# Optimization experiments

Measured on AMD Instinct MI355X. Metric: run time of the kernel, lower is better.

Reference implementation:

```python
import jax, jax.numpy as jnp
import numpy as np

N_NODES = 200000
D_IN = 256
D_OUT = 256
B = 4096
K1 = 25   # layer-1 fanout
K2 = 10   # layer-2 fanout
M = B * (1 + K2)  # layer-1 node set size: batch centers + their sampled neighbors


def setup_inputs() -> dict:
    key = jax.random.key(0)
    k1, k2, k3, k4, k5, k6 = jax.random.split(key, 6)
    features = jax.random.normal(k1, (N_NODES, D_IN), dtype=jnp.float32)
    # SageLayer weights: [out, 2*in] (concat path, gcn=False); small kaiming-like scale
    W1 = jax.random.normal(k2, (D_OUT, 2 * D_IN), dtype=jnp.float32) * 0.05
    W2 = jax.random.normal(k3, (D_OUT, 2 * D_OUT), dtype=jnp.float32) * 0.05
    nodes_batch = jax.random.randint(k4, (B,), 0, N_NODES, dtype=jnp.int64)
    neigh2 = jax.random.randint(k5, (B, K2), 0, N_NODES, dtype=jnp.int64)
    neigh1 = jax.random.randint(k6, (M, K1), 0, N_NODES, dtype=jnp.int64)
    return {"features": features, "W1": W1, "W2": W2,
            "nodes_batch": nodes_batch, "neigh2": neigh2, "neigh1": neigh1}


def reference(features, W1, W2, nodes_batch, neigh2, neigh1):
    # Layer-1 node set: centers first, then their sampled layer-2 neighbors.
    l1_nodes = jnp.concatenate([nodes_batch, neigh2.reshape(-1)])  # [M]
    # ---- layer 1: MEAN aggregate over K1 sampled neighbors (gather + mean) ----
    agg1 = jnp.mean(features[neigh1], axis=1)          # [M, K1, D_IN] -> [M, D_IN]
    self1 = features[l1_nodes]                         # [M, D_IN]
    # SageLayer: relu(W.mm(cat(self, agg).T)).T == relu(cat @ W.T)
    h1 = jax.nn.relu(jnp.concatenate([self1, agg1], axis=1) @ W1.T)  # [M, D_OUT]
    # ---- layer 2: centers are h1[:B]; neighbor embeddings are h1[B:] in blocks of K2 ----
    nb = nodes_batch.shape[0]
    agg2 = jnp.mean(h1[nb:].reshape(nb, -1, h1.shape[1]), axis=1)    # [B, D_OUT]
    h2 = jax.nn.relu(jnp.concatenate([h1[:nb], agg2], axis=1) @ W2.T)  # [B, D_OUT]
    return h2
```

## Files before the change

### kernel.cpp

```cpp
#include <hip/hip_runtime.h>
#include <hip/hip_bf16.h>

typedef __attribute__((ext_vector_type(8))) short bf16x8;
typedef __attribute__((ext_vector_type(4))) float f32x4;

#define B_SZ   4096
#define K1     25
#define K2     10
#define M_L1   45056
#define D      256
#define K_DIM  512

static __device__ __forceinline__ unsigned short f2bf(float f) {
    union { float f; unsigned u; } v; v.f = f;
    return (unsigned short)((v.u + 0x7fffu + ((v.u >> 16) & 1u)) >> 16);
}
static __device__ __forceinline__ float bf2f(unsigned short h) {
    union { unsigned u; float f; } v; v.u = ((unsigned)h) << 16;
    return v.f;
}

__global__ __launch_bounds__(256)
void convert_w(const float* __restrict__ W1, const float* __restrict__ W2,
               unsigned short* __restrict__ W1b, unsigned short* __restrict__ W2b) {
    const int i = blockIdx.x * 256 + threadIdx.x;
    W1b[i] = f2bf(W1[i]);
    W2b[i] = f2bf(W2[i]);
}

__global__ __launch_bounds__(256)
void agg1_kernel(const float* __restrict__ feat,
                 const int* __restrict__ nodes_batch,
                 const int* __restrict__ neigh2,
                 const int* __restrict__ neigh1,
                 unsigned short* __restrict__ X1) {
    const int wave = threadIdx.x >> 6;
    const int lane = threadIdx.x & 63;
    const int m = (blockIdx.x << 2) + wave;
    const int self_node = (m < B_SZ) ? nodes_batch[m] : neigh2[m - B_SZ];
    const float4 s = *(const float4*)(feat + (size_t)self_node * D + (lane << 2));
    float sx = 0.f, sy = 0.f, sz = 0.f, sw = 0.f;
    const int* nb = neigh1 + (size_t)m * K1;
    #pragma unroll
    for (int k = 0; k < K1; ++k) {
        const float4 v = *(const float4*)(feat + (size_t)nb[k] * D + (lane << 2));
        sx += v.x; sy += v.y; sz += v.z; sw += v.w;
    }
    const float inv = 1.0f / (float)K1;
    unsigned short* xr = X1 + (size_t)m * K_DIM;
    *(ushort4*)(xr + (lane << 2)) = make_ushort4(f2bf(s.x), f2bf(s.y), f2bf(s.z), f2bf(s.w));
    *(ushort4*)(xr + D + (lane << 2)) =
        make_ushort4(f2bf(sx * inv), f2bf(sy * inv), f2bf(sz * inv), f2bf(sw * inv));
}

__global__ __launch_bounds__(256)
void agg2_kernel(const unsigned short* __restrict__ h1,
                 unsigned short* __restrict__ X2) {
    const int wave = threadIdx.x >> 6;
    const int lane = threadIdx.x & 63;
    const int b = (blockIdx.x << 2) + wave;
    const ushort4 s = *(const ushort4*)(h1 + (size_t)b * D + (lane << 2));
    float sx = 0.f, sy = 0.f, sz = 0.f, sw = 0.f;
    #pragma unroll
    for (int k = 0; k < K2; ++k) {
        const ushort4 v = *(const ushort4*)(h1 + (size_t)(B_SZ + b * K2 + k) * D + (lane << 2));
        sx += bf2f(v.x); sy += bf2f(v.y); sz += bf2f(v.z); sw += bf2f(v.w);
    }
    const float inv = 1.0f / (float)K2;
    unsigned short* xr = X2 + (size_t)b * K_DIM;
    *(ushort4*)(xr + (lane << 2)) = s;
    *(ushort4*)(xr + D + (lane << 2)) =
        make_ushort4(f2bf(sx * inv), f2bf(sy * inv), f2bf(sz * inv), f2bf(sw * inv));
}

template<bool OUT_BF16>
__global__ __launch_bounds__(256)
void gemm_relu(const unsigned short* __restrict__ A,
               const unsigned short* __restrict__ W,
               void* __restrict__ Cout) {
    constexpr int LDA = 40;
    __shared__ unsigned short As[128 * LDA];
    __shared__ unsigned short Bs[128 * LDA];
    const int tid  = threadIdx.x;
    const int wave = tid >> 6, lane = tid & 63;
    const int quad = lane >> 4, l16 = lane & 15;
    const int wm = (wave >> 1) << 6;
    const int wn = (wave & 1) << 6;
    const size_t row0 = (size_t)blockIdx.x * 128;
    const size_t col0 = (size_t)blockIdx.y * 128;
    const int r0 = tid >> 2;
    const int c0 = (tid & 3) << 3;

    f32x4 acc[4][4];
    #pragma unroll
    for (int i = 0; i < 4; ++i)
        #pragma unroll
        for (int j = 0; j < 4; ++j)
            acc[i][j] = (f32x4){0.f, 0.f, 0.f, 0.f};

    const unsigned short* aBase = A + (row0 + r0) * K_DIM + c0;
    const unsigned short* wBase = W + (col0 + r0) * K_DIM + c0;

    for (int k0 = 0; k0 < K_DIM; k0 += 32) {
        __syncthreads();
        *(uint4*)&As[r0 * LDA + c0]        = *(const uint4*)(aBase + k0);
        *(uint4*)&As[(64 + r0) * LDA + c0] = *(const uint4*)(aBase + (size_t)64 * K_DIM + k0);
        *(uint4*)&Bs[r0 * LDA + c0]        = *(const uint4*)(wBase + k0);
        *(uint4*)&Bs[(64 + r0) * LDA + c0] = *(const uint4*)(wBase + (size_t)64 * K_DIM + k0);
        __syncthreads();
        bf16x8 af[4], bfr[4];
        #pragma unroll
        for (int i = 0; i < 4; ++i)
            af[i] = *(const bf16x8*)&As[(wm + i * 16 + l16) * LDA + quad * 8];
        #pragma unroll
        for (int i = 0; i < 4; ++i)
            bfr[i] = *(const bf16x8*)&Bs[(wn + i * 16 + l16) * LDA + quad * 8];
        #pragma unroll
        for (int mi = 0; mi < 4; ++mi)
            #pragma unroll
            for (int ni = 0; ni < 4; ++ni)
                acc[mi][ni] = __builtin_amdgcn_mfma_f32_16x16x32_bf16(
                    af[mi], bfr[ni], acc[mi][ni], 0, 0, 0);
    }

    #pragma unroll
    for (int mi = 0; mi < 4; ++mi) {
        #pragma unroll
        for (int ni = 0; ni < 4; ++ni) {
            #pragma unroll
            for (int r = 0; r < 4; ++r) {
                const size_t gm = row0 + wm + mi * 16 + quad * 4 + r;
                const size_t gn = col0 + wn + ni * 16 + l16;
                float v = acc[mi][ni][r];
                v = v > 0.f ? v : 0.f;
                if (OUT_BF16)
                    ((unsigned short*)Cout)[gm * D + gn] = f2bf(v);
                else
                    ((float*)Cout)[gm * D + gn] = v;
            }
        }
    }
}

extern "C" void kernel_launch(void* const* d_in, const int* in_sizes, int n_in,
                              void* d_out, int out_size, void* d_ws, size_t ws_size,
                              hipStream_t stream) {
    const float* feat        = (const float*)d_in[0];
    const float* W1          = (const float*)d_in[1];
    const float* W2          = (const float*)d_in[2];
    const int*   nodes_batch = (const int*)d_in[3];
    const int*   neigh2      = (const int*)d_in[4];
    const int*   neigh1      = (const int*)d_in[5];
    float* out = (float*)d_out;

    char* ws = (char*)d_ws;
    unsigned short* W1b = (unsigned short*)(ws);
    unsigned short* W2b = (unsigned short*)(ws + 262144);
    unsigned short* X1  = (unsigned short*)(ws + 524288);
    unsigned short* h1  = (unsigned short*)(ws + 524288 + 46137344);
    unsigned short* X2  = (unsigned short*)(ws + 524288 + 46137344 + 23068672);

    convert_w<<<512, 256, 0, stream>>>(W1, W2, W1b, W2b);
    agg1_kernel<<<M_L1 / 4, 256, 0, stream>>>(feat, nodes_batch, neigh2, neigh1, X1);
    gemm_relu<true><<<dim3(M_L1 / 128, 2), 256, 0, stream>>>(X1, W1b, h1);
    agg2_kernel<<<B_SZ / 4, 256, 0, stream>>>(h1, X2);
    gemm_relu<false><<<dim3(B_SZ / 128, 2), 256, 0, stream>>>(X2, W2b, out);
}
```

Before: 455.8 us.

## Convert feature table to bf16 and gather bf16 rows in agg1

Adds a pass that converts the whole fp32 feature table to bf16 in the workspace. agg1 then gathers 512-byte bf16 rows with half-waves, splits neighbors between the two halves, and combines the partial sums with a shuffle. The goal is to halve the bytes moved by the random gather. The cost is a full read of the 200k x 256 fp32 table and a write of its bf16 copy on every call, plus bf16 rounding of the neighbor values before averaging.

```diff
diff --git a/kernel.cpp b/kernel.cpp
--- a/kernel.cpp
+++ b/kernel.cpp
@@ -10,6 +10,7 @@
 #define M_L1   45056
 #define D      256
 #define K_DIM  512
+#define N_NODES 200000
 
 static __device__ __forceinline__ unsigned short f2bf(float f) {
     union { float f; unsigned u; } v; v.f = f;
@@ -18,6 +19,25 @@
 static __device__ __forceinline__ float bf2f(unsigned short h) {
     union { unsigned u; float f; } v; v.u = ((unsigned)h) << 16;
     return v.f;
+}
+static __device__ __forceinline__ float bfhi(unsigned u) {
+    union { unsigned u; float f; } v; v.u = u & 0xffff0000u;
+    return v.f;
+}
+static __device__ __forceinline__ float bflo(unsigned u) {
+    union { unsigned u; float f; } v; v.u = u << 16;
+    return v.f;
+}
+
+__global__ __launch_bounds__(256)
+void convert_feat(const float* __restrict__ f, unsigned short* __restrict__ fb) {
+    const size_t i = ((size_t)blockIdx.x * 256 + threadIdx.x) * 8;
+    const float4 a = *(const float4*)(f + i);
+    const float4 b = *(const float4*)(f + i + 4);
+    ushort4 r0 = make_ushort4(f2bf(a.x), f2bf(a.y), f2bf(a.z), f2bf(a.w));
+    ushort4 r1 = make_ushort4(f2bf(b.x), f2bf(b.y), f2bf(b.z), f2bf(b.w));
+    *(ushort4*)(fb + i) = r0;
+    *(ushort4*)(fb + i + 4) = r1;
 }
 
 __global__ __launch_bounds__(256)
@@ -29,28 +49,58 @@
 }
 
 __global__ __launch_bounds__(256)
-void agg1_kernel(const float* __restrict__ feat,
+void agg1_kernel(const unsigned short* __restrict__ featb,
                  const int* __restrict__ nodes_batch,
                  const int* __restrict__ neigh2,
                  const int* __restrict__ neigh1,
                  unsigned short* __restrict__ X1) {
     const int wave = threadIdx.x >> 6;
     const int lane = threadIdx.x & 63;
+    const int half = lane >> 5;
+    const int sl   = lane & 31;
     const int m = (blockIdx.x << 2) + wave;
     const int self_node = (m < B_SZ) ? nodes_batch[m] : neigh2[m - B_SZ];
-    const float4 s = *(const float4*)(feat + (size_t)self_node * D + (lane << 2));
-    float sx = 0.f, sy = 0.f, sz = 0.f, sw = 0.f;
     const int* nb = neigh1 + (size_t)m * K1;
-    #pragma unroll
-    for (int k = 0; k < K1; ++k) {
-        const float4 v = *(const float4*)(feat + (size_t)nb[k] * D + (lane << 2));
-        sx += v.x; sy += v.y; sz += v.z; sw += v.w;
-    }
-    const float inv = 1.0f / (float)K1;
+    const int e = sl << 3;
+
+    uint4 v[13];
+    #pragma unroll
+    for (int j = 0; j < 13; ++j) {
+        const int node = (j < 12) ? nb[2 * j + half]
+                                  : (half ? self_node : nb[24]);
+        v[j] = *(const uint4*)(featb + (size_t)node * D + e);
+    }
+
+    float acc[8] = {0.f, 0.f, 0.f, 0.f, 0.f, 0.f, 0.f, 0.f};
+    #pragma unroll
+    for (int j = 0; j < 12; ++j) {
+        acc[0] += bflo(v[j].x); acc[1] += bfhi(v[j].x);
+        acc[2] += bflo(v[j].y); acc[3] += bfhi(v[j].y);
+        acc[4] += bflo(v[j].z); acc[5] += bfhi(v[j].z);
+        acc[6] += bflo(v[j].w); acc[7] += bfhi(v[j].w);
+    }
+    if (half == 0) {
+        acc[0] += bflo(v[12].x); acc[1] += bfhi(v[12].x);
+        acc[2] += bflo(v[12].y); acc[3] += bfhi(v[12].y);
+        acc[4] += bflo(v[12].z); acc[5] += bfhi(v[12].z);
+        acc[6] += bflo(v[12].w); acc[7] += bfhi(v[12].w);
+    }
+    #pragma unroll
+    for (int i = 0; i < 8; ++i)
+        acc[i] += __shfl(acc[i], sl + 32);
+
     unsigned short* xr = X1 + (size_t)m * K_DIM;
-    *(ushort4*)(xr + (lane << 2)) = make_ushort4(f2bf(s.x), f2bf(s.y), f2bf(s.z), f2bf(s.w));
-    *(ushort4*)(xr + D + (lane << 2)) =
-        make_ushort4(f2bf(sx * inv), f2bf(sy * inv), f2bf(sz * inv), f2bf(sw * inv));
+    if (half == 0) {
+        const float inv = 1.0f / (float)K1;
+        ushort4 p0 = make_ushort4(f2bf(acc[0] * inv), f2bf(acc[1] * inv),
+                                  f2bf(acc[2] * inv), f2bf(acc[3] * inv));
+        ushort4 p1 = make_ushort4(f2bf(acc[4] * inv), f2bf(acc[5] * inv),
+                                  f2bf(acc[6] * inv), f2bf(acc[7] * inv));
+        *(ushort4*)(xr + D + e) = p0;
+        *(ushort4*)(xr + D + e + 4) = p1;
+    } else {
+        *(uint4*)(xr + e) = v[12];
+    }
 }
 
 __global__ __launch_bounds__(256)
@@ -154,14 +204,16 @@
     float* out = (float*)d_out;
 
     char* ws = (char*)d_ws;
-    unsigned short* W1b = (unsigned short*)(ws);
-    unsigned short* W2b = (unsigned short*)(ws + 262144);
-    unsigned short* X1  = (unsigned short*)(ws + 524288);
-    unsigned short* h1  = (unsigned short*)(ws + 524288 + 46137344);
-    unsigned short* X2  = (unsigned short*)(ws + 524288 + 46137344 + 23068672);
-
+    unsigned short* featb = (unsigned short*)(ws);
+    unsigned short* h1    = (unsigned short*)(ws);
+    unsigned short* X2    = (unsigned short*)(ws + 23068672);
+    unsigned short* X1    = (unsigned short*)(ws + 102400000);
+    unsigned short* W1b   = (unsigned short*)(ws + 102400000 + 46137344);
+    unsigned short* W2b   = (unsigned short*)(ws + 102400000 + 46137344 + 262144);
+
+    convert_feat<<<25000, 256, 0, stream>>>(feat, featb);
     convert_w<<<512, 256, 0, stream>>>(W1, W2, W1b, W2b);
-    agg1_kernel<<<M_L1 / 4, 256, 0, stream>>>(feat, nodes_batch, neigh2, neigh1, X1);
+    agg1_kernel<<<M_L1 / 4, 256, 0, stream>>>(featb, nodes_batch, neigh2, neigh1, X1);
     gemm_relu<true><<<dim3(M_L1 / 128, 2), 256, 0, stream>>>(X1, W1b, h1);
     agg2_kernel<<<B_SZ / 4, 256, 0, stream>>>(h1, X2);
     gemm_relu<false><<<dim3(B_SZ / 128, 2), 256, 0, stream>>>(X2, W2b, out);
```

After: 422.2 us. 7.4% less time.

## Gather layer-1 neighbor features from an FP8 copy of the feature table

Applied to the files above, without the earlier changes.

Each call now converts the full fp32 feature table to FP8 (e4m3) in the workspace. The layer-1 mean aggregation then gathers 4 bytes per lane per neighbor from that compact table instead of 16 bytes of fp32. Neighbor indices are loaded once per wave and broadcast with shuffles, and all 25 gathers are issued before accumulation so more loads are in flight. The aim is to cut random-gather traffic and let the smaller table sit in cache. The cost is an extra full-table conversion pass and a loss of precision in the aggregated means.

```diff
diff --git a/kernel.cpp b/kernel.cpp
--- a/kernel.cpp
+++ b/kernel.cpp
@@ -3,6 +3,7 @@
 
 typedef __attribute__((ext_vector_type(8))) short bf16x8;
 typedef __attribute__((ext_vector_type(4))) float f32x4;
+typedef __attribute__((ext_vector_type(2))) float f32x2;
 
 #define B_SZ   4096
 #define K1     25
@@ -10,6 +11,7 @@
 #define M_L1   45056
 #define D      256
 #define K_DIM  512
+#define N_NODES 200000
 
 static __device__ __forceinline__ unsigned short f2bf(float f) {
     union { float f; unsigned u; } v; v.f = f;
@@ -18,6 +20,20 @@
 static __device__ __forceinline__ float bf2f(unsigned short h) {
     union { unsigned u; float f; } v; v.u = ((unsigned)h) << 16;
     return v.f;
+}
+
+__global__ __launch_bounds__(256)
+void convert_fp8(const float* __restrict__ f, unsigned* __restrict__ f8) {
+    const size_t i = ((size_t)blockIdx.x * 256 + threadIdx.x) * 8;
+    const float4 a = *(const float4*)(f + i);
+    const float4 b = *(const float4*)(f + i + 4);
+    unsigned u0 = 0, u1 = 0;
+    u0 = __builtin_amdgcn_cvt_pk_fp8_f32(a.x, a.y, u0, false);
+    u0 = __builtin_amdgcn_cvt_pk_fp8_f32(a.z, a.w, u0, true);
+    u1 = __builtin_amdgcn_cvt_pk_fp8_f32(b.x, b.y, u1, false);
+    u1 = __builtin_amdgcn_cvt_pk_fp8_f32(b.z, b.w, u1, true);
+    uint2 r; r.x = u0; r.y = u1;
+    *(uint2*)(f8 + (i >> 2)) = r;
 }
 
 __global__ __launch_bounds__(256)
@@ -30,6 +46,7 @@
 
 __global__ __launch_bounds__(256)
 void agg1_kernel(const float* __restrict__ feat,
+                 const unsigned* __restrict__ f8,
                  const int* __restrict__ nodes_batch,
                  const int* __restrict__ neigh2,
                  const int* __restrict__ neigh1,
@@ -38,19 +55,33 @@
     const int lane = threadIdx.x & 63;
     const int m = (blockIdx.x << 2) + wave;
     const int self_node = (m < B_SZ) ? nodes_batch[m] : neigh2[m - B_SZ];
+    const int* nb = neigh1 + (size_t)m * K1;
+
+    int idxv = (lane < K1) ? nb[lane] : 0;
+
     const float4 s = *(const float4*)(feat + (size_t)self_node * D + (lane << 2));
-    float sx = 0.f, sy = 0.f, sz = 0.f, sw = 0.f;
-    const int* nb = neigh1 + (size_t)m * K1;
-    #pragma unroll
-    for (int k = 0; k < K1; ++k) {
-        const float4 v = *(const float4*)(feat + (size_t)nb[k] * D + (lane << 2));
-        sx += v.x; sy += v.y; sz += v.z; sw += v.w;
+
+    unsigned q[K1];
+    #pragma unroll
+    for (int j = 0; j < K1; ++j) {
+        const int node = __shfl(idxv, j);
+        q[j] = f8[(size_t)node * (D / 4) + lane];
+    }
+
+    float a0 = 0.f, a1 = 0.f, a2 = 0.f, a3 = 0.f;
+    #pragma unroll
+    for (int j = 0; j < K1; ++j) {
+        const f32x2 lo = __builtin_amdgcn_cvt_pk_f32_fp8(q[j], false);
+        const f32x2 hi = __builtin_amdgcn_cvt_pk_f32_fp8(q[j], true);
+        a0 += lo.x; a1 += lo.y; a2 += hi.x; a3 += hi.y;
     }
     const float inv = 1.0f / (float)K1;
+
     unsigned short* xr = X1 + (size_t)m * K_DIM;
-    *(ushort4*)(xr + (lane << 2)) = make_ushort4(f2bf(s.x), f2bf(s.y), f2bf(s.z), f2bf(s.w));
+    *(ushort4*)(xr + (lane << 2)) =
+        make_ushort4(f2bf(s.x), f2bf(s.y), f2bf(s.z), f2bf(s.w));
     *(ushort4*)(xr + D + (lane << 2)) =
-        make_ushort4(f2bf(sx * inv), f2bf(sy * inv), f2bf(sz * inv), f2bf(sw * inv));
+        make_ushort4(f2bf(a0 * inv), f2bf(a1 * inv), f2bf(a2 * inv), f2bf(a3 * inv));
 }
 
 __global__ __launch_bounds__(256)
@@ -154,14 +185,16 @@
     float* out = (float*)d_out;
 
     char* ws = (char*)d_ws;
-    unsigned short* W1b = (unsigned short*)(ws);
-    unsigned short* W2b = (unsigned short*)(ws + 262144);
-    unsigned short* X1  = (unsigned short*)(ws + 524288);
-    unsigned short* h1  = (unsigned short*)(ws + 524288 + 46137344);
-    unsigned short* X2  = (unsigned short*)(ws + 524288 + 46137344 + 23068672);
-
+    unsigned*       f8   = (unsigned*)(ws);
+    unsigned short* X1   = (unsigned short*)(ws + 51200000);
+    unsigned short* h1   = (unsigned short*)(ws + 51200000 + 46137344);
+    unsigned short* X2   = (unsigned short*)(ws + 51200000 + 46137344 + 23068672);
+    unsigned short* W1b  = (unsigned short*)(ws + 51200000 + 46137344 + 23068672 + 4194304);
+    unsigned short* W2b  = (unsigned short*)(ws + 51200000 + 46137344 + 23068672 + 4194304 + 262144);
+
+    convert_fp8<<<25000, 256, 0, stream>>>(feat, f8);
     convert_w<<<512, 256, 0, stream>>>(W1, W2, W1b, W2b);
-    agg1_kernel<<<M_L1 / 4, 256, 0, stream>>>(feat, nodes_batch, neigh2, neigh1, X1);
+    agg1_kernel<<<M_L1 / 4, 256, 0, stream>>>(feat, f8, nodes_batch, neigh2, neigh1, X1);
     gemm_relu<true><<<dim3(M_L1 / 128, 2), 256, 0, stream>>>(X1, W1b, h1);
     agg2_kernel<<<B_SZ / 4, 256, 0, stream>>>(h1, X2);
     gemm_relu<false><<<dim3(B_SZ / 128, 2), 256, 0, stream>>>(X2, W2b, out);
```

Result: faster. 381.4 us (-16.3%).
